# Kernel tuning notes

Measured on AMD Instinct MI355X. Metric: run time of the kernel, lower is better.

Reference implementation:

```python
import jax, jax.numpy as jnp
import numpy as np

B, S, H, N = 2, 2048, 1024, 16
D = H // N


def setup_inputs() -> dict:
    key = jax.random.key(0)
    k1, k2, k3 = jax.random.split(key, 3)
    # Xavier-uniform-ish init for projection weights
    lim_in = (6.0 / (H + 3 * H)) ** 0.5
    lim_out = (6.0 / (H + H)) ** 0.5
    return {
        "hidden_states": jax.random.normal(k1, (B, S, H), dtype=jnp.float32),
        "w_in": jax.random.uniform(k2, (3 * H, H), minval=-lim_in, maxval=lim_in, dtype=jnp.float32),
        "b_in": jnp.zeros((3 * H,), dtype=jnp.float32),
        "w_out": jax.random.uniform(k3, (H, H), minval=-lim_out, maxval=lim_out, dtype=jnp.float32),
        "b_out": jnp.zeros((H,), dtype=jnp.float32),
    }


def reference(hidden_states, w_in, b_in, w_out, b_out):
    b, s, h = hidden_states.shape
    qkv = hidden_states @ w_in.T + b_in  # [B,S,3H]
    q, k, v = jnp.split(qkv, 3, axis=-1)
    # [B,S,H] -> [B,N,S,D]
    def to_heads(x):
        return x.reshape(b, s, N, D).transpose(0, 2, 1, 3)
    q, k, v = to_heads(q), to_heads(k), to_heads(v)
    scale = D ** -0.5
    scores = jnp.einsum("bnqd,bnkd->bnqk", q, k) * scale  # [B,N,S,S]
    causal = jnp.triu(jnp.ones((s, s), dtype=bool), k=1)
    scores = jnp.where(causal, -jnp.inf, scores)
    attn = jax.nn.softmax(scores, axis=-1)
    out = jnp.einsum("bnqk,bnkd->bnqd", attn, v)  # [B,N,S,D]
    out = out.transpose(0, 2, 1, 3).reshape(b, s, h)
    return out @ w_out.T + b_out
```

## Files before the change

kernel.cpp:

```cpp
#include <hip/hip_runtime.h>
#include <hip/hip_bf16.h>

#define BB 2
#define SS 2048
#define HH 1024
#define NH 16
#define DD 64
#define H3 3072
#define MM (BB*SS)

typedef unsigned short u16;
typedef unsigned int u32;
typedef __attribute__((ext_vector_type(8))) short bf16x8;
typedef __attribute__((ext_vector_type(4))) float f32x4;
typedef __attribute__((ext_vector_type(16))) float f32x16;

__device__ __forceinline__ u16 f2bf(float f) {
    union { float f; u32 u; } v; v.f = f;
    u32 u = v.u;
    u += 0x7fffu + ((u >> 16) & 1u);
    return (u16)(u >> 16);
}
__device__ __forceinline__ float bf2f(u16 h) {
    union { u32 u; float f; } v; v.u = ((u32)h) << 16;
    return v.f;
}
__device__ __forceinline__ u32 pack2bf(float a, float b) {
    __hip_bfloat162 h = __float22bfloat162_rn(float2{a, b});
    u32 u; __builtin_memcpy(&u, &h, 4);
    return u;
}
__device__ __forceinline__ void gl_lds16(const void* g, void* l) {
    __builtin_amdgcn_global_load_lds(
        (const __attribute__((address_space(1))) u32*)g,
        (__attribute__((address_space(3))) u32*)l, 16, 0, 0);
}

__global__ void cvt3bf(const float4* __restrict__ s0, uint2* __restrict__ d0, int n0,
                       const float4* __restrict__ s1, uint2* __restrict__ d1, int n1,
                       const float4* __restrict__ s2, uint2* __restrict__ d2, int n2) {
    int i = blockIdx.x * blockDim.x + threadIdx.x;
    const int tot = n0 + n1 + n2;
    for (; i < tot; i += gridDim.x * blockDim.x) {
        const float4* s; uint2* d; int j;
        if (i < n0)            { s = s0; d = d0; j = i; }
        else if (i < n0 + n1)  { s = s1; d = d1; j = i - n0; }
        else                   { s = s2; d = d2; j = i - n0 - n1; }
        float4 v = s[j];
        uint2 o; o.x = pack2bf(v.x, v.y); o.y = pack2bf(v.z, v.w);
        d[j] = o;
    }
}

template<int BN, int MODE>
__global__ __launch_bounds__(256, 2)
void gemm_k2(const u16* __restrict__ A, const u16* __restrict__ Bbf,
             const u16* __restrict__ biasbf, void* __restrict__ Cptr,
             u16* __restrict__ Qo, u16* __restrict__ Ko, u16* __restrict__ Vto,
             int M, int Nn, int K)
{
    constexpr int NFR = BN / 32;
    __shared__ __align__(16) u16 Alds[128 * 32];
    __shared__ __align__(16) u16 Blds[BN * 32];
    const int tid = threadIdx.x;
    const int w = tid >> 6, lane = tid & 63, quad = lane >> 4, l16 = lane & 15;
    const int m0 = blockIdx.x * 128, n0 = blockIdx.y * BN;
    const int wm = w >> 1, wn = w & 1;
    const int rA4 = lane >> 2, c8b = (lane & 3) * 8;

    f32x4 acc[4][NFR] = {};

    for (int k0 = 0; k0 < K; k0 += 32) {
        __syncthreads();
#pragma unroll
        for (int q = 0; q < 2; ++q) {
            int row0 = w * 32 + q * 16;
            gl_lds16(&A[(size_t)(m0 + row0 + rA4) * K + k0 + c8b], &Alds[row0 * 32]);
        }
#pragma unroll
        for (int q = 0; q < BN / 64; ++q) {
            int row0 = w * (BN / 4) + q * 16;
            gl_lds16(&Bbf[(size_t)(n0 + row0 + rA4) * K + k0 + c8b], &Blds[row0 * 32]);
        }
        __syncthreads();

        bf16x8 af[4], bfr[NFR];
#pragma unroll
        for (int mi = 0; mi < 4; ++mi)
            af[mi] = *(const bf16x8*)&Alds[(wm * 64 + mi * 16 + l16) * 32 + quad * 8];
#pragma unroll
        for (int ni = 0; ni < NFR; ++ni)
            bfr[ni] = *(const bf16x8*)&Blds[(wn * (BN / 2) + ni * 16 + l16) * 32 + quad * 8];
#pragma unroll
        for (int mi = 0; mi < 4; ++mi)
#pragma unroll
            for (int ni = 0; ni < NFR; ++ni)
                acc[mi][ni] = __builtin_amdgcn_mfma_f32_16x16x32_bf16(
                    af[mi], bfr[ni], acc[mi][ni], 0, 0, 0);
    }

#pragma unroll
    for (int mi = 0; mi < 4; ++mi) {
        int row_b = m0 + wm * 64 + mi * 16 + quad * 4;
#pragma unroll
        for (int ni = 0; ni < NFR; ++ni) {
            int col = n0 + wn * (BN / 2) + ni * 16 + l16;
            float bv = bf2f(biasbf[col]);
            if constexpr (MODE == 1) {
#pragma unroll
                for (int i = 0; i < 4; ++i)
                    ((float*)Cptr)[(size_t)(row_b + i) * Nn + col] = acc[mi][ni][i] + bv;
            } else {
                if (col < 1024) {
#pragma unroll
                    for (int i = 0; i < 4; ++i)
                        Qo[(size_t)(row_b + i) * 1024 + col] =
                            f2bf((acc[mi][ni][i] + bv) * 0.125f);
                } else if (col < 2048) {
#pragma unroll
                    for (int i = 0; i < 4; ++i)
                        Ko[(size_t)(row_b + i) * 1024 + (col - 1024)] =
                            f2bf(acc[mi][ni][i] + bv);
                } else {
                    int d = col - 2048, hh = d >> 6, dd = d & 63;
                    int b = row_b >> 11, s = row_b & 2047;
                    u16 t0 = f2bf(acc[mi][ni][0] + bv), t1 = f2bf(acc[mi][ni][1] + bv);
                    u16 t2 = f2bf(acc[mi][ni][2] + bv), t3 = f2bf(acc[mi][ni][3] + bv);
                    uint2 pk; pk.x = (u32)t0 | ((u32)t1 << 16);
                    pk.y = (u32)t2 | ((u32)t3 << 16);
                    *(uint2*)&Vto[((size_t)((b * 16 + hh) * 64 + dd)) * 2048 + s] = pk;
                }
            }
        }
    }
}

__global__ __launch_bounds__(256, 2)
void attn_v6(const u16* __restrict__ Q, const u16* __restrict__ Kb,
             const u16* __restrict__ Vt, u16* __restrict__ attn_out) {
    const int pr = blockIdx.x, h = blockIdx.y, b = blockIdx.z;
    const int tid = threadIdx.x;
    const int w = tid >> 6, lane = tid & 63;
    const int l32 = lane & 31, h5 = lane >> 5;
    const int wq = w & 1;
    const int wp = w >> 1;

    __shared__ __align__(16) u16 Pb[4][32 * 72];
    __shared__ float Oc[2][32 * 68];
    __shared__ float lc[2][32];

    const u16* Qg = Q  + (size_t)(b * SS) * 1024 + h * 64;
    const u16* Kg = Kb + (size_t)(b * SS) * 1024 + h * 64;
    const u16* Vg = Vt + (size_t)((b * 16 + h) * 64) * 2048;

    for (int half = 0; half < 2; ++half) {
        const int qt = half ? pr : (31 - pr);
        const int q0 = qt * 64;
        const int qw = q0 + wq * 32;
        const int T = qt + 1;

        bf16x8 qf[4];
#pragma unroll
        for (int kt = 0; kt < 4; ++kt)
            qf[kt] = *(const bf16x8*)&Qg[(size_t)(qw + l32) * 1024 + kt * 16 + h5 * 8];

        f32x16 oacc[2] = {};
        float lp[16];
#pragma unroll
        for (int j = 0; j < 16; ++j) lp[j] = 0.f;

        for (int t = wp; t < T; t += 2) {
            const int kv0 = t * 64;
            f32x16 sacc[2] = {};
#pragma unroll
            for (int nt = 0; nt < 2; ++nt)
#pragma unroll
                for (int kt = 0; kt < 4; ++kt) {
                    bf16x8 kf = *(const bf16x8*)
                        &Kg[(size_t)(kv0 + nt * 32 + l32) * 1024 + kt * 16 + h5 * 8];
                    sacc[nt] = __builtin_amdgcn_mfma_f32_32x32x16_bf16(
                        qf[kt], kf, sacc[nt], 0, 0, 0);
                }
            if (t == qt) {
#pragma unroll
                for (int nt = 0; nt < 2; ++nt) {
                    int colg = kv0 + nt * 32 + l32;
#pragma unroll
                    for (int j = 0; j < 16; ++j) {
                        int rl = (j & 3) + 8 * (j >> 2) + 4 * h5;
                        float p = (colg <= qw + rl) ? __expf(sacc[nt][j]) : 0.f;
                        lp[j] += p;
                        Pb[w][rl * 72 + nt * 32 + l32] = f2bf(p);
                    }
                }
            } else {
#pragma unroll
                for (int nt = 0; nt < 2; ++nt)
#pragma unroll
                    for (int j = 0; j < 16; ++j) {
                        int rl = (j & 3) + 8 * (j >> 2) + 4 * h5;
                        float p = __expf(sacc[nt][j]);
                        lp[j] += p;
                        Pb[w][rl * 72 + nt * 32 + l32] = f2bf(p);
                    }
            }
#pragma unroll
            for (int kt = 0; kt < 4; ++kt) {
                bf16x8 pa = *(const bf16x8*)&Pb[w][l32 * 72 + kt * 16 + h5 * 8];
#pragma unroll
                for (int nt = 0; nt < 2; ++nt) {
                    bf16x8 vf = *(const bf16x8*)
                        &Vg[(size_t)(nt * 32 + l32) * 2048 + kv0 + kt * 16 + h5 * 8];
                    oacc[nt] = __builtin_amdgcn_mfma_f32_32x32x16_bf16(
                        pa, vf, oacc[nt], 0, 0, 0);
                }
            }
        }

#pragma unroll
        for (int j = 0; j < 16; ++j)
#pragma unroll
            for (int s = 1; s < 32; s <<= 1)
                lp[j] += __shfl_xor(lp[j], s, 64);

        if (wp == 1) {
#pragma unroll
            for (int nt = 0; nt < 2; ++nt)
#pragma unroll
                for (int j = 0; j < 16; ++j) {
                    int rl = (j & 3) + 8 * (j >> 2) + 4 * h5;
                    Oc[wq][rl * 68 + nt * 32 + l32] = oacc[nt][j];
                }
            if (l32 == 0)
#pragma unroll
                for (int j = 0; j < 16; ++j) {
                    int rl = (j & 3) + 8 * (j >> 2) + 4 * h5;
                    lc[wq][rl] = lp[j];
                }
        }
        __syncthreads();
        if (wp == 0) {
            u16* ob = attn_out + (size_t)(b * SS + qw) * 1024 + h * 64;
#pragma unroll
            for (int j = 0; j < 16; ++j) {
                int rl = (j & 3) + 8 * (j >> 2) + 4 * h5;
                float linv = 1.0f / (lp[j] + lc[wq][rl]);
#pragma unroll
                for (int nt = 0; nt < 2; ++nt) {
                    float v = (oacc[nt][j] + Oc[wq][rl * 68 + nt * 32 + l32]) * linv;
                    ob[(size_t)rl * 1024 + nt * 32 + l32] = f2bf(v);
                }
            }
        }
        __syncthreads();
    }
}

extern "C" void kernel_launch(void* const* d_in, const int* in_sizes, int n_in,
                              void* d_out, int out_size, void* d_ws, size_t ws_size,
                              hipStream_t stream) {
    const float* hidden = (const float*)d_in[0];
    const float* w_in   = (const float*)d_in[1];
    const float* b_in   = (const float*)d_in[2];
    const float* w_out  = (const float*)d_in[3];
    const float* b_out  = (const float*)d_in[4];
    float* out = (float*)d_out;

    char* ws = (char*)d_ws;
    u16* hid_bf  = (u16*)d_out;
    u16* wi_bf   = (u16*)ws;
    u16* bi_bf   = (u16*)(ws + 6291456);
    u16* attn_ws = (u16*)ws;
    u16* Qbuf    = (u16*)(ws + 8388608);
    u16* wo_bf   = (u16*)(ws + 8388608);
    u16* bo_bf   = (u16*)(ws + 8388608 + 2097152);
    u16* Kbuf    = (u16*)(ws + 16777216);
    u16* Vtbuf   = (u16*)(ws + 25165824);

    cvt3bf<<<dim3(2048), dim3(256), 0, stream>>>(
        (const float4*)hidden, (uint2*)hid_bf, 1048576,
        (const float4*)w_in,   (uint2*)wi_bf,  786432,
        (const float4*)b_in,   (uint2*)bi_bf,  768);
    gemm_k2<128, 2><<<dim3(32, 24), dim3(256), 0, stream>>>(
        hid_bf, wi_bf, bi_bf, nullptr, Qbuf, Kbuf, Vtbuf, MM, H3, HH);
    attn_v6<<<dim3(16, NH, BB), dim3(256), 0, stream>>>(
        Qbuf, Kbuf, Vtbuf, attn_ws);
    cvt3bf<<<dim3(512), dim3(256), 0, stream>>>(
        (const float4*)w_out, (uint2*)wo_bf, 262144,
        (const float4*)b_out, (uint2*)bo_bf, 256,
        nullptr, nullptr, 0);
    gemm_k2<64, 1><<<dim3(32, 16), dim3(256), 0, stream>>>(
        attn_ws, wo_bf, bo_bf, out, nullptr, nullptr, nullptr, MM, HH, HH);
}
```

Measured before the change: 215.3 us.

## Store Q/K/V in MFMA-fragment-swizzled layout and split attention into 32-row query blocks

The QKV GEMM epilogue now writes Q, K and V per head in a layout that matches the MFMA fragment order, so each lane's bf16x8 load in attention reads a contiguous 512-byte chunk per wave. Before, those loads were strided across 1024-element rows. The attention kernel moves to 128-thread blocks, each owning a 32-row query tile and splitting the KV tiles between two waves, with twice as many blocks in the grid. This aims at better coalescing and more parallelism. In exchange, the epilogue writes become scattered 2-byte stores, and the causal mask now uses a last-tile test that covers a partially masked 64-wide tile.

```diff
diff --git a/kernel.cpp b/kernel.cpp
--- a/kernel.cpp
+++ b/kernel.cpp
@@ -51,6 +51,7 @@
         d[j] = o;
     }
 }
+
 
 template<int BN, int MODE>
 __global__ __launch_bounds__(256, 2)
@@ -111,58 +112,61 @@
                 for (int i = 0; i < 4; ++i)
                     ((float*)Cptr)[(size_t)(row_b + i) * Nn + col] = acc[mi][ni][i] + bv;
             } else {
-                if (col < 1024) {
-#pragma unroll
-                    for (int i = 0; i < 4; ++i)
-                        Qo[(size_t)(row_b + i) * 1024 + col] =
-                            f2bf((acc[mi][ni][i] + bv) * 0.125f);
-                } else if (col < 2048) {
-#pragma unroll
-                    for (int i = 0; i < 4; ++i)
-                        Ko[(size_t)(row_b + i) * 1024 + (col - 1024)] =
-                            f2bf(acc[mi][ni][i] + bv);
+                const int b = row_b >> 11, srow = row_b & 2047;
+                if (col < 2048) {
+                    int d = col & 1023, hh = d >> 6, dd = d & 63;
+                    int kt = dd >> 4, h5w = (dd >> 3) & 1, j = dd & 7;
+                    u16* dst = (col < 1024 ? Qo : Ko) + (size_t)(b * 16 + hh) * 131072;
+                    float sc = (col < 1024) ? 0.125f : 1.0f;
+#pragma unroll
+                    for (int i = 0; i < 4; ++i) {
+                        int s = srow + i;
+                        dst[(((s >> 5) * 4 + kt) * 2 + h5w) * 256 + (s & 31) * 8 + j] =
+                            f2bf((acc[mi][ni][i] + bv) * sc);
+                    }
                 } else {
                     int d = col - 2048, hh = d >> 6, dd = d & 63;
-                    int b = row_b >> 11, s = row_b & 2047;
+                    int t2 = (srow >> 6) * 2 + (dd >> 5);
+                    int kt = (srow >> 4) & 3, h5w = (srow >> 3) & 1;
+                    int l32w = dd & 31, j0 = srow & 7;
+                    u16* vb = Vto + (size_t)(b * 16 + hh) * 131072;
                     u16 t0 = f2bf(acc[mi][ni][0] + bv), t1 = f2bf(acc[mi][ni][1] + bv);
-                    u16 t2 = f2bf(acc[mi][ni][2] + bv), t3 = f2bf(acc[mi][ni][3] + bv);
+                    u16 t2v = f2bf(acc[mi][ni][2] + bv), t3 = f2bf(acc[mi][ni][3] + bv);
                     uint2 pk; pk.x = (u32)t0 | ((u32)t1 << 16);
-                    pk.y = (u32)t2 | ((u32)t3 << 16);
-                    *(uint2*)&Vto[((size_t)((b * 16 + hh) * 64 + dd)) * 2048 + s] = pk;
-                }
-            }
-        }
-    }
-}
-
-__global__ __launch_bounds__(256, 2)
-void attn_v6(const u16* __restrict__ Q, const u16* __restrict__ Kb,
-             const u16* __restrict__ Vt, u16* __restrict__ attn_out) {
+                    pk.y = (u32)t2v | ((u32)t3 << 16);
+                    *(uint2*)&vb[((t2 * 4 + kt) * 2 + h5w) * 256 + l32w * 8 + j0] = pk;
+                }
+            }
+        }
+    }
+}
+
+__global__ __launch_bounds__(128, 2)
+void attn_v7(const u16* __restrict__ Qswz, const u16* __restrict__ Kswz,
+             const u16* __restrict__ Vswz, u16* __restrict__ attn_out) {
     const int pr = blockIdx.x, h = blockIdx.y, b = blockIdx.z;
     const int tid = threadIdx.x;
-    const int w = tid >> 6, lane = tid & 63;
+    const int wp = tid >> 6, lane = tid & 63;
     const int l32 = lane & 31, h5 = lane >> 5;
-    const int wq = w & 1;
-    const int wp = w >> 1;
-
-    __shared__ __align__(16) u16 Pb[4][32 * 72];
-    __shared__ float Oc[2][32 * 68];
-    __shared__ float lc[2][32];
-
-    const u16* Qg = Q  + (size_t)(b * SS) * 1024 + h * 64;
-    const u16* Kg = Kb + (size_t)(b * SS) * 1024 + h * 64;
-    const u16* Vg = Vt + (size_t)((b * 16 + h) * 64) * 2048;
+
+    __shared__ __align__(16) u16 Pb[2][32 * 72];
+    __shared__ float Oc[32 * 68];
+    __shared__ float lc[32];
+
+    const u16* Qg = Qswz + (size_t)(b * 16 + h) * 131072;
+    const u16* Kg = Kswz + (size_t)(b * 16 + h) * 131072;
+    const u16* Vg = Vswz + (size_t)(b * 16 + h) * 131072;
+    const int fo = h5 * 256 + l32 * 8;
 
     for (int half = 0; half < 2; ++half) {
-        const int qt = half ? pr : (31 - pr);
-        const int q0 = qt * 64;
-        const int qw = q0 + wq * 32;
-        const int T = qt + 1;
+        const int qt = half ? pr : (63 - pr);
+        const int qw = qt * 32;
+        const int T = (qt >> 1) + 1;
 
         bf16x8 qf[4];
 #pragma unroll
         for (int kt = 0; kt < 4; ++kt)
-            qf[kt] = *(const bf16x8*)&Qg[(size_t)(qw + l32) * 1024 + kt * 16 + h5 * 8];
+            qf[kt] = *(const bf16x8*)&Qg[((qt * 4 + kt) * 2) * 256 + fo];
 
         f32x16 oacc[2] = {};
         float lp[16];
@@ -170,47 +174,36 @@
         for (int j = 0; j < 16; ++j) lp[j] = 0.f;
 
         for (int t = wp; t < T; t += 2) {
-            const int kv0 = t * 64;
             f32x16 sacc[2] = {};
 #pragma unroll
-            for (int nt = 0; nt < 2; ++nt)
+            for (int nt = 0; nt < 2; ++nt) {
+                const int t2 = t * 2 + nt;
 #pragma unroll
                 for (int kt = 0; kt < 4; ++kt) {
-                    bf16x8 kf = *(const bf16x8*)
-                        &Kg[(size_t)(kv0 + nt * 32 + l32) * 1024 + kt * 16 + h5 * 8];
+                    bf16x8 kf = *(const bf16x8*)&Kg[(t2 * 4 + kt) * 512 + fo];
                     sacc[nt] = __builtin_amdgcn_mfma_f32_32x32x16_bf16(
                         qf[kt], kf, sacc[nt], 0, 0, 0);
                 }
-            if (t == qt) {
+            }
+            const bool lastt = (t == T - 1);
+#pragma unroll
+            for (int nt = 0; nt < 2; ++nt) {
+                int colg = t * 64 + nt * 32 + l32;
+#pragma unroll
+                for (int j = 0; j < 16; ++j) {
+                    int rl = (j & 3) + 8 * (j >> 2) + 4 * h5;
+                    float p = (!lastt || colg <= qw + rl) ? __expf(sacc[nt][j]) : 0.f;
+                    lp[j] += p;
+                    Pb[wp][rl * 72 + nt * 32 + l32] = f2bf(p);
+                }
+            }
+#pragma unroll
+            for (int kt = 0; kt < 4; ++kt) {
+                bf16x8 pa = *(const bf16x8*)&Pb[wp][l32 * 72 + kt * 16 + h5 * 8];
 #pragma unroll
                 for (int nt = 0; nt < 2; ++nt) {
-                    int colg = kv0 + nt * 32 + l32;
-#pragma unroll
-                    for (int j = 0; j < 16; ++j) {
-                        int rl = (j & 3) + 8 * (j >> 2) + 4 * h5;
-                        float p = (colg <= qw + rl) ? __expf(sacc[nt][j]) : 0.f;
-                        lp[j] += p;
-                        Pb[w][rl * 72 + nt * 32 + l32] = f2bf(p);
-                    }
-                }
-            } else {
-#pragma unroll
-                for (int nt = 0; nt < 2; ++nt)
-#pragma unroll
-                    for (int j = 0; j < 16; ++j) {
-                        int rl = (j & 3) + 8 * (j >> 2) + 4 * h5;
-                        float p = __expf(sacc[nt][j]);
-                        lp[j] += p;
-                        Pb[w][rl * 72 + nt * 32 + l32] = f2bf(p);
-                    }
-            }
-#pragma unroll
-            for (int kt = 0; kt < 4; ++kt) {
-                bf16x8 pa = *(const bf16x8*)&Pb[w][l32 * 72 + kt * 16 + h5 * 8];
-#pragma unroll
-                for (int nt = 0; nt < 2; ++nt) {
-                    bf16x8 vf = *(const bf16x8*)
-                        &Vg[(size_t)(nt * 32 + l32) * 2048 + kv0 + kt * 16 + h5 * 8];
+                    const int t2 = t * 2 + nt;
+                    bf16x8 vf = *(const bf16x8*)&Vg[(t2 * 4 + kt) * 512 + fo];
                     oacc[nt] = __builtin_amdgcn_mfma_f32_32x32x16_bf16(
                         pa, vf, oacc[nt], 0, 0, 0);
                 }
@@ -229,13 +222,13 @@
 #pragma unroll
                 for (int j = 0; j < 16; ++j) {
                     int rl = (j & 3) + 8 * (j >> 2) + 4 * h5;
-                    Oc[wq][rl * 68 + nt * 32 + l32] = oacc[nt][j];
+                    Oc[rl * 68 + nt * 32 + l32] = oacc[nt][j];
                 }
             if (l32 == 0)
 #pragma unroll
                 for (int j = 0; j < 16; ++j) {
                     int rl = (j & 3) + 8 * (j >> 2) + 4 * h5;
-                    lc[wq][rl] = lp[j];
+                    lc[rl] = lp[j];
                 }
         }
         __syncthreads();
@@ -244,10 +237,10 @@
 #pragma unroll
             for (int j = 0; j < 16; ++j) {
                 int rl = (j & 3) + 8 * (j >> 2) + 4 * h5;
-                float linv = 1.0f / (lp[j] + lc[wq][rl]);
+                float linv = 1.0f / (lp[j] + lc[rl]);
 #pragma unroll
                 for (int nt = 0; nt < 2; ++nt) {
-                    float v = (oacc[nt][j] + Oc[wq][rl * 68 + nt * 32 + l32]) * linv;
+                    float v = (oacc[nt][j] + Oc[rl * 68 + nt * 32 + l32]) * linv;
                     ob[(size_t)rl * 1024 + nt * 32 + l32] = f2bf(v);
                 }
             }
@@ -283,7 +276,7 @@
         (const float4*)b_in,   (uint2*)bi_bf,  768);
     gemm_k2<128, 2><<<dim3(32, 24), dim3(256), 0, stream>>>(
         hid_bf, wi_bf, bi_bf, nullptr, Qbuf, Kbuf, Vtbuf, MM, H3, HH);
-    attn_v6<<<dim3(16, NH, BB), dim3(256), 0, stream>>>(
+    attn_v7<<<dim3(32, NH, BB), dim3(128), 0, stream>>>(
         Qbuf, Kbuf, Vtbuf, attn_ws);
     cvt3bf<<<dim3(512), dim3(256), 0, stream>>>(
         (const float4*)w_out, (uint2*)wo_bf, 262144,
```

New measurement: 189.8 us. 1.13x faster.
